# Performance work log

Hardware: AMD Instinct MI355X
Metric: run time of the kernel (lower is better)

The kernel has to match this reference:

```python
import jax, jax.numpy as jnp
import numpy as np

L_Q, B, Q = 512, 256, 512
IN, H, A = 512, 1024, 512
L_H = 512


def _xavier(key, shape):
    fan_out, fan_in = shape
    lim = (6.0 / (fan_in + fan_out)) ** 0.5
    return jax.random.uniform(key, shape, minval=-lim, maxval=lim, dtype=jnp.float32)


def setup_inputs() -> dict:
    key = jax.random.key(0)
    ks = jax.random.split(key, 12)
    return {
        "query_data": jax.random.normal(ks[0], (L_Q, B, Q), dtype=jnp.float32),
        "query_mask": jnp.ones((L_Q, B), dtype=jnp.float32),
        "input": jax.random.normal(ks[1], (B, IN), dtype=jnp.float32),
        "parent_index": jax.random.randint(ks[2], (B,), 0, L_H),
        "history": jax.random.normal(ks[3], (L_H, B, H), dtype=jnp.float32),
        "h0": jax.random.normal(ks[4], (B, H), dtype=jnp.float32),
        "c0": jax.random.normal(ks[5], (B, H), dtype=jnp.float32),
        "W_ih": _xavier(ks[6], (4 * H, IN + Q + H)),
        "W_hh": _xavier(ks[7], (4 * H, H)),
        "b_ih": jnp.zeros((4 * H,), dtype=jnp.float32),
        "b_hh": jnp.zeros((4 * H,), dtype=jnp.float32),
        "att1_w": _xavier(ks[8], (A, Q + H)),
        "att1_b": jnp.zeros((A,), dtype=jnp.float32),
        "att2_w": _xavier(ks[9], (1, A)),
        "att2_b": jnp.zeros((1,), dtype=jnp.float32),
    }


def reference(query_data, query_mask, input, parent_index, history, h0, c0,
              W_ih, W_hh, b_ih, b_hh, att1_w, att1_b, att2_w, att2_b):
    L_q, Bn, _ = query_data.shape
    # attention: concat broadcast h0 with query, two linears + tanh
    h_ctx = jnp.broadcast_to(h0[None], (L_q, Bn, h0.shape[1]))
    att = jnp.concatenate([h_ctx, query_data], axis=2)          # (L_q, B, H+Q)
    att_hidden = jnp.tanh(att @ att1_w.T + att1_b)               # (L_q, B, A)
    att_raw = (att_hidden @ att2_w.T + att2_b)[..., 0]           # (L_q, B)
    # manual masked softmax over L_q (faithful: max taken before masking)
    e = jnp.exp(att_raw - jnp.max(att_raw, axis=0, keepdims=True)) * query_mask
    w = e / jnp.sum(e, axis=0, keepdims=True)                    # (L_q, B)
    ctx_vec = jnp.sum(query_data * w[..., None], axis=0)         # (B, Q)
    # query_history: gather instead of one-hot matmul
    h_parent = history[parent_index, jnp.arange(Bn)]             # (B, H)
    # LSTMCell (dropout=0 -> identity); torch gate order i, f, g, o
    x = jnp.concatenate([input, ctx_vec, h_parent], axis=1)      # (B, IN+Q+H)
    gates = x @ W_ih.T + b_ih + h0 @ W_hh.T + b_hh               # (B, 4H)
    i, f, g, o = jnp.split(gates, 4, axis=1)
    c1 = jax.nn.sigmoid(f) * c0 + jax.nn.sigmoid(i) * jnp.tanh(g)
    h1 = jax.nn.sigmoid(o) * jnp.tanh(c1)
    return ctx_vec, h1, c1
```

## Files before the change

kernel.cpp:

```cpp
#include <hip/hip_runtime.h>
#include <hip/hip_bf16.h>


typedef short bf16x8 __attribute__((ext_vector_type(8)));
typedef float f32x4 __attribute__((ext_vector_type(4)));
typedef unsigned short u16x4 __attribute__((ext_vector_type(4)));

__device__ __forceinline__ unsigned short f2bf(float f) {
  unsigned int u = __builtin_bit_cast(unsigned int, f);
  u += 0x7fffu + ((u >> 16) & 1u);
  return (unsigned short)(u >> 16);
}
__device__ __forceinline__ float bf2f(unsigned short u) {
  unsigned int x = (unsigned int)u << 16;
  return __builtin_bit_cast(float, x);
}
__device__ __forceinline__ float fast_tanh(float x) {
  float e = __expf(2.0f * x);
  return 1.0f - 2.0f / (e + 1.0f);
}
__device__ __forceinline__ float fast_sig(float x) {
  return 1.0f / (1.0f + __expf(-x));
}
__device__ __forceinline__ f32x4 mfma16(bf16x8 a, bf16x8 b, f32x4 c) {
  return __builtin_amdgcn_mfma_f32_16x16x32_bf16(a, b, c, 0, 0, 0);
}

__global__ void k_prep(const float* __restrict__ a1w, const float* __restrict__ h0,
                       unsigned short* __restrict__ wqf, float* __restrict__ part1) {
  __shared__ float sh[4096], swt[4096];
  int bx = blockIdx.x;
  if (bx < 128) {
    int g = bx * 256 + threadIdx.x;
    int lane = g & 63, frag = g >> 6;
    int ab = frag >> 4, ksf = frag & 15;
    int a = ab * 16 + (lane & 15);
    int k = ksf * 32 + (lane >> 4) * 8;
    const float* src = a1w + (size_t)a * 1536 + 1024 + k;
    float4 v0 = *reinterpret_cast<const float4*>(src);
    float4 v1 = *reinterpret_cast<const float4*>(src + 4);
    unsigned short* dst = wqf + ((size_t)frag * 64 + lane) * 8;
    *(u16x4*)dst       = u16x4{ f2bf(v0.x), f2bf(v0.y), f2bf(v0.z), f2bf(v0.w) };
    *(u16x4*)(dst + 4) = u16x4{ f2bf(v1.x), f2bf(v1.y), f2bf(v1.z), f2bf(v1.w) };
    return;
  }
  int blk = bx - 128;
  int at = blk & 7, bt = (blk >> 3) & 3, ksp = blk >> 5;
  int a0 = at * 64, b0 = bt * 64, kbase = ksp * 128;
  int t = threadIdx.x;
  int ta = t & 15, tb = t >> 4;
  float acc[4][4] = {};
  for (int half = 0; half < 2; half++) {
    int k0 = kbase + half * 64;
    for (int i = 0; i < 4; i++) {
      int u = i * 256 + t;
      int row = u >> 4, c4 = (u & 15) << 2;
      float4 vh = *reinterpret_cast<const float4*>(h0 + (size_t)(b0 + row) * 1024 + k0 + c4);
      float4 vw = *reinterpret_cast<const float4*>(a1w + (size_t)(a0 + row) * 1536 + k0 + c4);
      int off = (row * 256 + c4 * 4) ^ ((row & 7) << 4);
      *(float4*)((char*)sh + off) = vh;
      *(float4*)((char*)swt + off) = vw;
    }
    __syncthreads();
    for (int k4 = 0; k4 < 16; k4++) {
      float4 hv[4], wv[4];
#pragma unroll
      for (int i = 0; i < 4; i++) {
        int rh = tb + 16 * i;
        hv[i] = *(const float4*)((char*)sh + ((rh * 256 + k4 * 16) ^ ((rh & 7) << 4)));
        int ra = ta + 16 * i;
        wv[i] = *(const float4*)((char*)swt + ((ra * 256 + k4 * 16) ^ ((ra & 7) << 4)));
      }
#pragma unroll
      for (int i = 0; i < 4; i++)
#pragma unroll
        for (int j = 0; j < 4; j++)
          acc[i][j] += hv[i].x * wv[j].x + hv[i].y * wv[j].y +
                       hv[i].z * wv[j].z + hv[i].w * wv[j].w;
    }
    __syncthreads();
  }
  float* dst = part1 + (size_t)ksp * 131072;
#pragma unroll
  for (int i = 0; i < 4; i++)
#pragma unroll
    for (int j = 0; j < 4; j++)
      dst[(size_t)(b0 + tb + 16 * i) * 512 + a0 + ta + 16 * j] = acc[i][j];
}

__global__ void k_base2(const float* __restrict__ part1, const float* __restrict__ a1b,
                        float* __restrict__ base) {
  int idx = blockIdx.x * 256 + threadIdx.x;
  float s = a1b[idx & 511];
  for (int ks = 0; ks < 8; ks++) s += part1[(size_t)ks * 131072 + idx];
  base[idx] = s;
}

__global__ __launch_bounds__(512, 2) void k_attgemm(
    const float* __restrict__ qd, const unsigned short* __restrict__ wqf,
    const float* __restrict__ base, const float* __restrict__ w2,
    const float* __restrict__ mask, float* __restrict__ nump,
    float* __restrict__ denp) {
  extern __shared__ char smem[];
  float* sRed = (float*)(smem + 65536);
  float* e_lds = (float*)(smem + 65536 + 2048);
  int t = threadIdx.x;
  int bt = blockIdx.x & 15, lt = blockIdx.x >> 4;
  int b0 = bt * 16, l0 = lt * 16;
  int lane = t & 63, lr = lane & 15, lh = lane >> 4;
  int w = t >> 6;
  int b_own = t >> 5, q0 = (t & 31) * 16;
  float ctx_acc[16] = {};
  float den_acc = 0.0f;
  for (int ls = 0; ls < 4; ls++) {
    int l_base = l0 + ls * 4;
    for (int i = 0; i < 16; i++) {
      int u = i * 512 + t;
      int row = u >> 7, c4 = (u & 127) << 2;
      float4 v = *reinterpret_cast<const float4*>(
          qd + ((size_t)(l_base + (row >> 4)) * 256 + b0 + (row & 15)) * 512 + c4);
      int loff = (row * 1024 + c4 * 2) ^ ((row & 7) << 4);
      *(u16x4*)(smem + loff) = u16x4{ f2bf(v.x), f2bf(v.y), f2bf(v.z), f2bf(v.w) };
    }
    __syncthreads();
    f32x4 acc[4][4] = {};
#pragma unroll 4
    for (int ks = 0; ks < 16; ks++) {
      bf16x8 aF[4], bF[4];
#pragma unroll
      for (int mi = 0; mi < 4; mi++) {
        int row = mi * 16 + lr;
        int off = (row * 1024 + (ks * 32 + lh * 8) * 2) ^ ((row & 7) << 4);
        aF[mi] = *(const bf16x8*)(smem + off);
      }
#pragma unroll
      for (int ni = 0; ni < 4; ni++) {
        int ab = w * 4 + ni;
        bF[ni] = *(const bf16x8*)(wqf + ((size_t)(ab * 16 + ks) * 64 + lane) * 8);
      }
#pragma unroll
      for (int mi = 0; mi < 4; mi++)
#pragma unroll
        for (int ni = 0; ni < 4; ni++)
          acc[mi][ni] = mfma16(aF[mi], bF[ni], acc[mi][ni]);
    }
    float rs[4][4] = {};
#pragma unroll
    for (int ni = 0; ni < 4; ni++) {
      int a = w * 64 + ni * 16 + lr;
      float w2v = w2[a];
#pragma unroll
      for (int mi = 0; mi < 4; mi++)
#pragma unroll
        for (int r = 0; r < 4; r++) {
          int b = b0 + lh * 4 + r;
          float val = acc[mi][ni][r] + base[(size_t)b * 512 + a];
          rs[mi][r] += fast_tanh(val) * w2v;
        }
    }
#pragma unroll
    for (int mi = 0; mi < 4; mi++)
#pragma unroll
      for (int r = 0; r < 4; r++) {
        float v = rs[mi][r];
        v += __shfl_xor(v, 1); v += __shfl_xor(v, 2);
        v += __shfl_xor(v, 4); v += __shfl_xor(v, 8);
        rs[mi][r] = v;
      }
    if (lr == 0)
#pragma unroll
      for (int mi = 0; mi < 4; mi++)
#pragma unroll
        for (int r = 0; r < 4; r++)
          sRed[w * 64 + mi * 16 + lh * 4 + r] = rs[mi][r];
    __syncthreads();
    if (t < 64) {
      float araw = 0.0f;
#pragma unroll
      for (int j = 0; j < 8; j++) araw += sRed[j * 64 + t];
      int l = l_base + (t >> 4), b = b0 + (t & 15);
      e_lds[t] = __expf(araw) * mask[(size_t)l * 256 + b];
    }
    __syncthreads();
#pragma unroll
    for (int li = 0; li < 4; li++) {
      int row = li * 16 + b_own;
      float e = e_lds[row];
      if ((t & 31) == 0) den_acc += e;
      int sw = (row & 7) << 4;
      bf16x8 v0 = *(const bf16x8*)(smem + ((row * 1024 + q0 * 2) ^ sw));
      bf16x8 v1 = *(const bf16x8*)(smem + ((row * 1024 + q0 * 2 + 16) ^ sw));
#pragma unroll
      for (int j = 0; j < 8; j++) {
        ctx_acc[j]     += e * bf2f((unsigned short)v0[j]);
        ctx_acc[8 + j] += e * bf2f((unsigned short)v1[j]);
      }
    }
    __syncthreads();
  }
  float* dst = nump + ((size_t)lt * 256 + b0 + b_own) * 512 + q0;
#pragma unroll
  for (int j = 0; j < 4; j++)
    *reinterpret_cast<float4*>(dst + j * 4) =
        float4{ ctx_acc[j * 4], ctx_acc[j * 4 + 1], ctx_acc[j * 4 + 2], ctx_acc[j * 4 + 3] };
  if ((t & 31) == 0) denp[lt * 256 + b0 + b_own] = den_acc;
}

__global__ void k_ctxred(const float* __restrict__ nump, const float* __restrict__ denp,
                         float* __restrict__ outF) {
  int idx = blockIdx.x * 256 + threadIdx.x;
  int b = idx >> 9;
  float s = 0.0f, d = 0.0f;
#pragma unroll 8
  for (int lt = 0; lt < 32; lt++) {
    s += nump[(size_t)lt * 131072 + idx];
    d += denp[lt * 256 + b];
  }
  outF[idx] = s / d;
}

__global__ void k_xf(const float* __restrict__ inp, const float* __restrict__ ctx,
                     const float* __restrict__ hist, const int* __restrict__ pidx,
                     const float* __restrict__ h0, unsigned short* __restrict__ xf) {
  int g = blockIdx.x * 256 + threadIdx.x;
  int lane = g & 63, frag = g >> 6;
  int mb = frag / 96, kstep = frag % 96;
  int b = mb * 16 + (lane & 15);
  int k = kstep * 32 + (lane >> 4) * 8;
  const float* src;
  if (k < 512)       src = inp  + (size_t)b * 512 + k;
  else if (k < 1024) src = ctx  + (size_t)b * 512 + (k - 512);
  else if (k < 2048) src = hist + ((size_t)pidx[b] * 256 + b) * 1024 + (k - 1024);
  else               src = h0   + (size_t)b * 1024 + (k - 2048);
  float4 v0 = *reinterpret_cast<const float4*>(src);
  float4 v1 = *reinterpret_cast<const float4*>(src + 4);
  unsigned short* dst = xf + ((size_t)frag * 64 + lane) * 8;
  *(u16x4*)dst       = u16x4{ f2bf(v0.x), f2bf(v0.y), f2bf(v0.z), f2bf(v0.w) };
  *(u16x4*)(dst + 4) = u16x4{ f2bf(v1.x), f2bf(v1.y), f2bf(v1.z), f2bf(v1.w) };
}

__global__ __launch_bounds__(256, 4) void k_gates(
    const unsigned short* __restrict__ xf, const float* __restrict__ Wih,
    const float* __restrict__ Whh, float* __restrict__ part) {
  int blk = blockIdx.x;
  int nt = blk & 127, ksp = blk >> 7;
  int n0 = nt * 32, kbeg = ksp * 768;
  int t = threadIdx.x;
  int lane = t & 63, lr = lane & 15, lh = lane >> 4;
  int w = t >> 6;
  f32x4 acc[4][2] = {};
#pragma unroll 2
  for (int ks = 0; ks < 24; ks++) {
    int k0 = kbeg + ks * 32;
    int kstep = k0 >> 5;
    bf16x8 aF[4], bF[2];
#pragma unroll
    for (int mi = 0; mi < 4; mi++) {
      int mb = w * 4 + mi;
      aF[mi] = *(const bf16x8*)(xf + ((size_t)(mb * 96 + kstep) * 64 + lane) * 8);
    }
    const float* Wp; int ldw, kk;
    if (k0 < 2048) { Wp = Wih; ldw = 2048; kk = k0; }
    else           { Wp = Whh; ldw = 1024; kk = k0 - 2048; }
#pragma unroll
    for (int ni = 0; ni < 2; ni++) {
      int j = n0 + ni * 16 + lr;
      const float* src = Wp + (size_t)j * ldw + kk + lh * 8;
      float4 v0 = *reinterpret_cast<const float4*>(src);
      float4 v1 = *reinterpret_cast<const float4*>(src + 4);
      bf16x8 bv;
      bv[0] = (short)f2bf(v0.x); bv[1] = (short)f2bf(v0.y);
      bv[2] = (short)f2bf(v0.z); bv[3] = (short)f2bf(v0.w);
      bv[4] = (short)f2bf(v1.x); bv[5] = (short)f2bf(v1.y);
      bv[6] = (short)f2bf(v1.z); bv[7] = (short)f2bf(v1.w);
      bF[ni] = bv;
    }
#pragma unroll
    for (int mi = 0; mi < 4; mi++)
#pragma unroll
      for (int ni = 0; ni < 2; ni++)
        acc[mi][ni] = mfma16(aF[mi], bF[ni], acc[mi][ni]);
  }
  float* dst = part + (size_t)ksp * (256 * 4096);
#pragma unroll
  for (int mi = 0; mi < 4; mi++)
#pragma unroll
    for (int ni = 0; ni < 2; ni++)
#pragma unroll
      for (int r = 0; r < 4; r++) {
        int b = w * 64 + mi * 16 + lh * 4 + r;
        int j = n0 + ni * 16 + lr;
        dst[(size_t)b * 4096 + j] = acc[mi][ni][r];
      }
}

__global__ void k_lstm(const float* __restrict__ part, const float* __restrict__ bih,
                       const float* __restrict__ bhh, const float* __restrict__ c0,
                       float* __restrict__ out) {
  int idx = blockIdx.x * 256 + threadIdx.x;
  int h = idx & 1023;
  int b = idx >> 10;
  const float* p = part + (size_t)b * 4096;
  float gi = bih[h] + bhh[h];
  float gf = bih[1024 + h] + bhh[1024 + h];
  float gg = bih[2048 + h] + bhh[2048 + h];
  float go = bih[3072 + h] + bhh[3072 + h];
#pragma unroll
  for (int ks = 0; ks < 4; ks++) {
    const float* q = p + (size_t)ks * 1048576;
    gi += q[h]; gf += q[1024 + h]; gg += q[2048 + h]; go += q[3072 + h];
  }
  float c = fast_sig(gf) * c0[idx] + fast_sig(gi) * fast_tanh(gg);
  float hv = fast_sig(go) * fast_tanh(c);
  out[131072 + idx] = hv;
  out[393216 + idx] = c;
}

extern "C" void kernel_launch(void* const* d_in, const int* in_sizes, int n_in,
                              void* d_out, int out_size, void* d_ws, size_t ws_size,
                              hipStream_t stream) {
  const float* qd    = (const float*)d_in[0];
  const float* qmask = (const float*)d_in[1];
  const float* inp   = (const float*)d_in[2];
  const int*   pidx  = (const int*)d_in[3];
  const float* hist  = (const float*)d_in[4];
  const float* h0    = (const float*)d_in[5];
  const float* c0    = (const float*)d_in[6];
  const float* Wih   = (const float*)d_in[7];
  const float* Whh   = (const float*)d_in[8];
  const float* bih   = (const float*)d_in[9];
  const float* bhh   = (const float*)d_in[10];
  const float* a1w   = (const float*)d_in[11];
  const float* a1b   = (const float*)d_in[12];
  const float* a2w   = (const float*)d_in[13];
  float* outF = (float*)d_out;

  char* ws = (char*)d_ws;
  unsigned short* wqf  = (unsigned short*)(ws);
  float*          base = (float*)(ws + 524288);
  float*          p1   = (float*)(ws + 1048576);
  unsigned short* xf   = (unsigned short*)(ws + 5242880);
  float*          denp = (float*)(ws + 6815744);
  float*          nump = (float*)(ws + 8388608);
  float*          pg   = (float*)(ws + 25165824);

  (void)hipFuncSetAttribute((const void*)k_attgemm,
                            hipFuncAttributeMaxDynamicSharedMemorySize, 67840);

  k_prep   <<<384,  256, 0, stream>>>(a1w, h0, wqf, p1);
  k_base2  <<<512,  256, 0, stream>>>(p1, a1b, base);
  k_attgemm<<<512,  512, 67840, stream>>>(qd, wqf, base, a2w, qmask, nump, denp);
  k_ctxred <<<512,  256, 0, stream>>>(nump, denp, outF);
  k_xf     <<<384,  256, 0, stream>>>(inp, outF, hist, pidx, h0, xf);
  k_gates  <<<512,  256, 0, stream>>>(xf, Wih, Whh, pg);
  k_lstm   <<<1024, 256, 0, stream>>>(pg, bih, bhh, c0, outF);
}
```

Measured before the change: 249.6 us.

## Double-buffer query tiles in attention GEMM and fuse context reduction into xf packing

The attention GEMM kernel now keeps two LDS buffers and prefetches the next 4-row query chunk from global memory into registers while the MFMA loop runs on the current chunk, writing it to the other buffer afterwards. This aims to hide global load latency behind compute. Dynamic LDS doubles to about 130 KB, which with launch_bounds(512,2) likely cuts occupancy to one block per CU. Separately, the context-vector reduction kernel is removed and folded into k_xf, which sums the partial numerators and denominators directly, saving one launch and one global round trip.

```diff
diff --git a/kernel.cpp b/kernel.cpp
--- a/kernel.cpp
+++ b/kernel.cpp
@@ -102,8 +102,8 @@
     const float* __restrict__ mask, float* __restrict__ nump,
     float* __restrict__ denp) {
   extern __shared__ char smem[];
-  float* sRed = (float*)(smem + 65536);
-  float* e_lds = (float*)(smem + 65536 + 2048);
+  float* sRed = (float*)(smem + 131072);
+  float* e_lds = (float*)(smem + 131072 + 2048);
   int t = threadIdx.x;
   int bt = blockIdx.x & 15, lt = blockIdx.x >> 4;
   int b0 = bt * 16, l0 = lt * 16;
@@ -112,37 +112,64 @@
   int b_own = t >> 5, q0 = (t & 31) * 16;
   float ctx_acc[16] = {};
   float den_acc = 0.0f;
+
+  for (int i = 0; i < 16; i++) {
+    int u = i * 512 + t;
+    int row = u >> 7, c4 = (u & 127) << 2;
+    float4 v = *reinterpret_cast<const float4*>(
+        qd + ((size_t)(l0 + (row >> 4)) * 256 + b0 + (row & 15)) * 512 + c4);
+    int loff = (row * 1024 + c4 * 2) ^ ((row & 7) << 4);
+    *(u16x4*)(smem + loff) = u16x4{ f2bf(v.x), f2bf(v.y), f2bf(v.z), f2bf(v.w) };
+  }
+  __syncthreads();
+
   for (int ls = 0; ls < 4; ls++) {
-    int l_base = l0 + ls * 4;
-    for (int i = 0; i < 16; i++) {
-      int u = i * 512 + t;
-      int row = u >> 7, c4 = (u & 127) << 2;
-      float4 v = *reinterpret_cast<const float4*>(
-          qd + ((size_t)(l_base + (row >> 4)) * 256 + b0 + (row & 15)) * 512 + c4);
-      int loff = (row * 1024 + c4 * 2) ^ ((row & 7) << 4);
-      *(u16x4*)(smem + loff) = u16x4{ f2bf(v.x), f2bf(v.y), f2bf(v.z), f2bf(v.w) };
-    }
-    __syncthreads();
+    char* cb = smem + (size_t)(ls & 1) * 65536;
+    char* nb = smem + (size_t)((ls + 1) & 1) * 65536;
+    int lb1 = l0 + (ls + 1) * 4;
     f32x4 acc[4][4] = {};
-#pragma unroll 4
-    for (int ks = 0; ks < 16; ks++) {
-      bf16x8 aF[4], bF[4];
-#pragma unroll
-      for (int mi = 0; mi < 4; mi++) {
-        int row = mi * 16 + lr;
-        int off = (row * 1024 + (ks * 32 + lh * 8) * 2) ^ ((row & 7) << 4);
-        aF[mi] = *(const bf16x8*)(smem + off);
-      }
-#pragma unroll
-      for (int ni = 0; ni < 4; ni++) {
-        int ab = w * 4 + ni;
-        bF[ni] = *(const bf16x8*)(wqf + ((size_t)(ab * 16 + ks) * 64 + lane) * 8);
-      }
-#pragma unroll
-      for (int mi = 0; mi < 4; mi++)
-#pragma unroll
-        for (int ni = 0; ni < 4; ni++)
-          acc[mi][ni] = mfma16(aF[mi], bF[ni], acc[mi][ni]);
+    float4 sv[4];
+    for (int ks4 = 0; ks4 < 4; ks4++) {
+      if (ls < 3) {
+#pragma unroll
+        for (int i = 0; i < 4; i++) {
+          int u = (ks4 * 4 + i) * 512 + t;
+          int row = u >> 7, c4 = (u & 127) << 2;
+          sv[i] = *reinterpret_cast<const float4*>(
+              qd + ((size_t)(lb1 + (row >> 4)) * 256 + b0 + (row & 15)) * 512 + c4);
+        }
+      }
+#pragma unroll
+      for (int ksl = 0; ksl < 4; ksl++) {
+        int ks = ks4 * 4 + ksl;
+        bf16x8 aF[4], bF[4];
+#pragma unroll
+        for (int mi = 0; mi < 4; mi++) {
+          int row = mi * 16 + lr;
+          int off = (row * 1024 + (ks * 32 + lh * 8) * 2) ^ ((row & 7) << 4);
+          aF[mi] = *(const bf16x8*)(cb + off);
+        }
+#pragma unroll
+        for (int ni = 0; ni < 4; ni++) {
+          int ab = w * 4 + ni;
+          bF[ni] = *(const bf16x8*)(wqf + ((size_t)(ab * 16 + ks) * 64 + lane) * 8);
+        }
+#pragma unroll
+        for (int mi = 0; mi < 4; mi++)
+#pragma unroll
+          for (int ni = 0; ni < 4; ni++)
+            acc[mi][ni] = mfma16(aF[mi], bF[ni], acc[mi][ni]);
+      }
+      if (ls < 3) {
+#pragma unroll
+        for (int i = 0; i < 4; i++) {
+          int u = (ks4 * 4 + i) * 512 + t;
+          int row = u >> 7, c4 = (u & 127) << 2;
+          int loff = (row * 1024 + c4 * 2) ^ ((row & 7) << 4);
+          *(u16x4*)(nb + loff) =
+              u16x4{ f2bf(sv[i].x), f2bf(sv[i].y), f2bf(sv[i].z), f2bf(sv[i].w) };
+        }
+      }
     }
     float rs[4][4] = {};
 #pragma unroll
@@ -178,7 +205,7 @@
       float araw = 0.0f;
 #pragma unroll
       for (int j = 0; j < 8; j++) araw += sRed[j * 64 + t];
-      int l = l_base + (t >> 4), b = b0 + (t & 15);
+      int l = l0 + ls * 4 + (t >> 4), b = b0 + (t & 15);
       e_lds[t] = __expf(araw) * mask[(size_t)l * 256 + b];
     }
     __syncthreads();
@@ -188,8 +215,8 @@
       float e = e_lds[row];
       if ((t & 31) == 0) den_acc += e;
       int sw = (row & 7) << 4;
-      bf16x8 v0 = *(const bf16x8*)(smem + ((row * 1024 + q0 * 2) ^ sw));
-      bf16x8 v1 = *(const bf16x8*)(smem + ((row * 1024 + q0 * 2 + 16) ^ sw));
+      bf16x8 v0 = *(const bf16x8*)(cb + ((row * 1024 + q0 * 2) ^ sw));
+      bf16x8 v1 = *(const bf16x8*)(cb + ((row * 1024 + q0 * 2 + 16) ^ sw));
 #pragma unroll
       for (int j = 0; j < 8; j++) {
         ctx_acc[j]     += e * bf2f((unsigned short)v0[j]);
@@ -206,34 +233,42 @@
   if ((t & 31) == 0) denp[lt * 256 + b0 + b_own] = den_acc;
 }
 
-__global__ void k_ctxred(const float* __restrict__ nump, const float* __restrict__ denp,
-                         float* __restrict__ outF) {
-  int idx = blockIdx.x * 256 + threadIdx.x;
-  int b = idx >> 9;
-  float s = 0.0f, d = 0.0f;
-#pragma unroll 8
-  for (int lt = 0; lt < 32; lt++) {
-    s += nump[(size_t)lt * 131072 + idx];
-    d += denp[lt * 256 + b];
-  }
-  outF[idx] = s / d;
-}
-
-__global__ void k_xf(const float* __restrict__ inp, const float* __restrict__ ctx,
-                     const float* __restrict__ hist, const int* __restrict__ pidx,
-                     const float* __restrict__ h0, unsigned short* __restrict__ xf) {
+__global__ void k_xf(const float* __restrict__ inp, const float* __restrict__ nump,
+                     const float* __restrict__ denp, const float* __restrict__ hist,
+                     const int* __restrict__ pidx, const float* __restrict__ h0,
+                     unsigned short* __restrict__ xf, float* __restrict__ outF) {
   int g = blockIdx.x * 256 + threadIdx.x;
   int lane = g & 63, frag = g >> 6;
   int mb = frag / 96, kstep = frag % 96;
   int b = mb * 16 + (lane & 15);
   int k = kstep * 32 + (lane >> 4) * 8;
-  const float* src;
-  if (k < 512)       src = inp  + (size_t)b * 512 + k;
-  else if (k < 1024) src = ctx  + (size_t)b * 512 + (k - 512);
-  else if (k < 2048) src = hist + ((size_t)pidx[b] * 256 + b) * 1024 + (k - 1024);
-  else               src = h0   + (size_t)b * 1024 + (k - 2048);
-  float4 v0 = *reinterpret_cast<const float4*>(src);
-  float4 v1 = *reinterpret_cast<const float4*>(src + 4);
+  float4 v0, v1;
+  if (k >= 512 && k < 1024) {
+    int q0 = k - 512;
+    float d = 0.0f;
+    v0 = float4{0, 0, 0, 0}; v1 = float4{0, 0, 0, 0};
+#pragma unroll 4
+    for (int lt = 0; lt < 32; lt++) {
+      d += denp[lt * 256 + b];
+      const float* p = nump + ((size_t)lt * 256 + b) * 512 + q0;
+      float4 a0 = *reinterpret_cast<const float4*>(p);
+      float4 a1 = *reinterpret_cast<const float4*>(p + 4);
+      v0.x += a0.x; v0.y += a0.y; v0.z += a0.z; v0.w += a0.w;
+      v1.x += a1.x; v1.y += a1.y; v1.z += a1.z; v1.w += a1.w;
+    }
+    float inv = 1.0f / d;
+    v0.x *= inv; v0.y *= inv; v0.z *= inv; v0.w *= inv;
+    v1.x *= inv; v1.y *= inv; v1.z *= inv; v1.w *= inv;
+    *reinterpret_cast<float4*>(outF + (size_t)b * 512 + q0) = v0;
+    *reinterpret_cast<float4*>(outF + (size_t)b * 512 + q0 + 4) = v1;
+  } else {
+    const float* src;
+    if (k < 512)       src = inp  + (size_t)b * 512 + k;
+    else if (k < 2048) src = hist + ((size_t)pidx[b] * 256 + b) * 1024 + (k - 1024);
+    else               src = h0   + (size_t)b * 1024 + (k - 2048);
+    v0 = *reinterpret_cast<const float4*>(src);
+    v1 = *reinterpret_cast<const float4*>(src + 4);
+  }
   unsigned short* dst = xf + ((size_t)frag * 64 + lane) * 8;
   *(u16x4*)dst       = u16x4{ f2bf(v0.x), f2bf(v0.y), f2bf(v0.z), f2bf(v0.w) };
   *(u16x4*)(dst + 4) = u16x4{ f2bf(v1.x), f2bf(v1.y), f2bf(v1.z), f2bf(v1.w) };
@@ -345,13 +380,12 @@
   float*          pg   = (float*)(ws + 25165824);
 
   (void)hipFuncSetAttribute((const void*)k_attgemm,
-                            hipFuncAttributeMaxDynamicSharedMemorySize, 67840);
+                            hipFuncAttributeMaxDynamicSharedMemorySize, 133376);
 
   k_prep   <<<384,  256, 0, stream>>>(a1w, h0, wqf, p1);
   k_base2  <<<512,  256, 0, stream>>>(p1, a1b, base);
-  k_attgemm<<<512,  512, 67840, stream>>>(qd, wqf, base, a2w, qmask, nump, denp);
-  k_ctxred <<<512,  256, 0, stream>>>(nump, denp, outF);
-  k_xf     <<<384,  256, 0, stream>>>(inp, outF, hist, pidx, h0, xf);
+  k_attgemm<<<512,  512, 133376, stream>>>(qd, wqf, base, a2w, qmask, nump, denp);
+  k_xf     <<<384,  256, 0, stream>>>(inp, nump, denp, hist, pidx, h0, xf, outF);
   k_gates  <<<512,  256, 0, stream>>>(xf, Wih, Whh, pg);
   k_lstm   <<<1024, 256, 0, stream>>>(pg, bih, bhh, c0, outF);
 }
```

New measurement: 237.9 us. 4.7% less time.
